# Performance work log

Hardware: AMD Instinct MI355X
Metric: run time of the kernel (lower is better)

## Reference

```python
import jax, jax.numpy as jnp
import numpy as np

B, N, K = 1, 100000, 16
C_IN, C_ADD, C_MID = 64, 16, 16
IN_F, OUT_F = (C_IN + C_ADD) * C_MID, 256


def setup_inputs() -> dict:
    key = jax.random.key(0)
    ks = jax.random.split(key, 8)
    return {
        "input_features": jax.random.normal(ks[0], (B, N, C_IN), dtype=jnp.float32),
        "neighbor_inds": jax.random.randint(ks[1], (B, N, K), 0, N, dtype=jnp.int32),
        "inverse_neighbors": jax.random.randint(ks[2], (B, N * K), 0, N, dtype=jnp.int32),
        "inverse_k": jax.random.randint(ks[3], (B, N + 1), 0, K, dtype=jnp.int32),
        "inverse_idx": jax.random.randint(ks[4], (B, N * K), 0, N * K, dtype=jnp.int32),
        "weightnet": jax.random.normal(ks[5], (B, N, K, C_MID), dtype=jnp.float32),
        "additional_features": jax.random.normal(ks[6], (B, N, K, C_ADD), dtype=jnp.float32),
        "linear_weights": jax.random.normal(ks[7], (OUT_F, IN_F), dtype=jnp.float32) * 0.02,
        "linear_bias": jnp.zeros((OUT_F,), dtype=jnp.float32),
    }


def reference(input_features, neighbor_inds, inverse_neighbors, inverse_k,
              inverse_idx, weightnet, additional_features,
              linear_weights, linear_bias):
    # Gather neighbor features: [B, N, K, C_in]
    gathered = jax.vmap(lambda f, idx: f[idx])(input_features, neighbor_inds)
    # Concatenate extra per-neighbor features: [B, N, K, C_in + C_add]
    feat = jnp.concatenate([gathered, additional_features], axis=-1)
    # WeightNet-weighted reduction over neighbors: [B, N, C, C_mid]
    pconv = jnp.einsum("bnkc,bnkm->bncm", feat, weightnet)
    pconv = pconv.reshape(pconv.shape[0], pconv.shape[1], -1)  # [B, N, C*C_mid]
    # Fused linear projection
    return pconv @ linear_weights.T + linear_bias
```

## Files before the change

kernel.cpp:

```cpp
#include <hip/hip_runtime.h>

#define NPTS 100000
#define PB 64
#define NBLK ((NPTS + PB - 1) / PB)
#define INF 1280
#define OUTF 256

using short8 = __attribute__((ext_vector_type(8))) short;
using f32x4  = __attribute__((ext_vector_type(4))) float;

__device__ __forceinline__ unsigned short f2bf(float x) {
  unsigned u = __float_as_uint(x);
  return (unsigned short)((u + 0x7FFFu + ((u >> 16) & 1u)) >> 16);
}

__global__ void k_prep(const float* __restrict__ in_f, unsigned short* __restrict__ inbf) {
  int i = blockIdx.x * 256 + threadIdx.x;
  if (i < 1600000) {
    float4 v = ((const float4*)in_f)[i];
    ushort4 o;
    o.x = f2bf(v.x); o.y = f2bf(v.y); o.z = f2bf(v.z); o.w = f2bf(v.w);
    ((ushort4*)inbf)[i] = o;
  }
}

__global__ void k_wconv(const float* __restrict__ W, unsigned short* __restrict__ Wb) {
  int g = blockIdx.x * 256 + threadIdx.x;
  int j = g & 7;
  int col = (g >> 3) & 15;
  int ks = (g >> 7) & 31;
  int rest = g >> 12;
  int ct = rest % 5, nt = rest / 5;
  int kh = ks * 8 + j;
  int m = kh >> 4, ci = kh & 15;
  Wb[g] = f2bf(W[(nt * 16 + col) * INF + (ct * 16 + ci) * 16 + m]);
}

__global__ __launch_bounds__(512, 4) void k_fused(
    const unsigned short* __restrict__ inbf, const int* __restrict__ nbr,
    const float* __restrict__ wn_g, const float* __restrict__ add_f,
    const unsigned short* __restrict__ Wb, const float* __restrict__ bias,
    float* __restrict__ out)
{
  __shared__ __align__(16) unsigned char sA[PB * 528];
  __shared__ __align__(16) unsigned char sW[PB * 512];
  __shared__ int s_nbr[PB * 16];

  const int t = threadIdx.x;
  const int w = t >> 6, lane = t & 63;
  const int g16 = lane >> 4;
  const int c16 = lane & 15;
  const long p0 = (long)blockIdx.x * PB;

  for (int i = t; i < PB * 16; i += 512) {
    long pp = p0 + (i >> 4); if (pp >= NPTS) pp = NPTS - 1;
    s_nbr[i] = nbr[pp * 16 + (i & 15)];
  }
#pragma unroll
  for (int it = 0; it < 8; ++it) {
    int flat4 = it * 512 + t;
    int p = flat4 >> 6, k = (flat4 >> 2) & 15, m4 = (flat4 & 3) * 4;
    long pp = p0 + p; if (pp >= NPTS) pp = NPTS - 1;
    float4 v = *(const float4*)(wn_g + pp * 256 + k * 16 + m4);
    unsigned short* wb = (unsigned short*)(sW + p * 512 + k * 2);
    wb[(m4 + 0) * 16] = f2bf(v.x);
    wb[(m4 + 1) * 16] = f2bf(v.y);
    wb[(m4 + 2) * 16] = f2bf(v.z);
    wb[(m4 + 3) * 16] = f2bf(v.w);
  }
  __syncthreads();

  f32x4 acc[2][4];
#pragma unroll
  for (int a = 0; a < 2; ++a)
#pragma unroll
    for (int b = 0; b < 4; ++b) acc[a][b] = (f32x4){0.f, 0.f, 0.f, 0.f};

  const int rt0 = (w & 1) * 2;
  const int nt0 = (w >> 1) * 4;

  for (int ct = 0; ct < 5; ++ct) {
#pragma unroll 2
    for (int i = 0; i < 8; ++i) {
      int p = w * 8 + i;
      long pp = p0 + p; if (pp >= NPTS) pp = NPTS - 1;
      short8 af = (short8){0, 0, 0, 0, 0, 0, 0, 0};
      short8 bf = (short8){0, 0, 0, 0, 0, 0, 0, 0};
      if (g16 < 2) {
        bf = *(const short8*)(sW + p * 512 + c16 * 32 + g16 * 16);
        int4 i0 = *(const int4*)&s_nbr[p * 16 + g16 * 8];
        int4 i1 = *(const int4*)&s_nbr[p * 16 + g16 * 8 + 4];
        unsigned short a8[8];
        if (ct < 4) {
          a8[0] = inbf[(long)i0.x * 64 + ct * 16 + c16];
          a8[1] = inbf[(long)i0.y * 64 + ct * 16 + c16];
          a8[2] = inbf[(long)i0.z * 64 + ct * 16 + c16];
          a8[3] = inbf[(long)i0.w * 64 + ct * 16 + c16];
          a8[4] = inbf[(long)i1.x * 64 + ct * 16 + c16];
          a8[5] = inbf[(long)i1.y * 64 + ct * 16 + c16];
          a8[6] = inbf[(long)i1.z * 64 + ct * 16 + c16];
          a8[7] = inbf[(long)i1.w * 64 + ct * 16 + c16];
        } else {
#pragma unroll
          for (int j = 0; j < 8; ++j)
            a8[j] = f2bf(add_f[(pp * 16 + g16 * 8 + j) * 16 + c16]);
        }
#pragma unroll
        for (int j = 0; j < 8; ++j) ((unsigned short*)&af)[j] = a8[j];
      }
      f32x4 d = __builtin_amdgcn_mfma_f32_16x16x32_bf16(af, bf, (f32x4){0.f, 0.f, 0.f, 0.f}, 0, 0, 0);
      unsigned lo = (unsigned)f2bf(d[0]) | ((unsigned)f2bf(d[1]) << 16);
      unsigned hi = (unsigned)f2bf(d[2]) | ((unsigned)f2bf(d[3]) << 16);
      *(uint2*)(sA + p * 528 + c16 * 32 + g16 * 8) = make_uint2(lo, hi);
    }
    __syncthreads();

#pragma unroll
    for (int kl = 0; kl < 8; ++kl) {
      short8 a0 = *(const short8*)(sA + (rt0 * 16 + c16) * 528 + kl * 64 + g16 * 16);
      short8 a1 = *(const short8*)(sA + ((rt0 + 1) * 16 + c16) * 528 + kl * 64 + g16 * 16);
#pragma unroll
      for (int ntl = 0; ntl < 4; ++ntl) {
        int nt = nt0 + ntl;
        short8 b = *(const short8*)(Wb + (((long)(nt * 5 + ct) * 32 + kl * 4 + g16) * 16 + c16) * 8);
        acc[0][ntl] = __builtin_amdgcn_mfma_f32_16x16x32_bf16(a0, b, acc[0][ntl], 0, 0, 0);
        acc[1][ntl] = __builtin_amdgcn_mfma_f32_16x16x32_bf16(a1, b, acc[1][ntl], 0, 0, 0);
      }
    }
    __syncthreads();
  }

#pragma unroll
  for (int ntl = 0; ntl < 4; ++ntl) {
    int n = nt0 * 16 + ntl * 16 + c16;
    float bv = bias[n];
#pragma unroll
    for (int rr = 0; rr < 2; ++rr) {
      long prow = p0 + (rt0 + rr) * 16 + g16 * 4;
#pragma unroll
      for (int r = 0; r < 4; ++r) {
        if (prow + r < NPTS) out[(prow + r) * 256 + n] = acc[rr][ntl][r] + bv;
      }
    }
  }
}

extern "C" void kernel_launch(void* const* d_in, const int* in_sizes, int n_in,
                              void* d_out, int out_size, void* d_ws, size_t ws_size,
                              hipStream_t stream) {
  const float* in_f  = (const float*)d_in[0];
  const int*   nbr   = (const int*)d_in[1];
  const float* wn    = (const float*)d_in[5];
  const float* add_f = (const float*)d_in[6];
  const float* W     = (const float*)d_in[7];
  const float* bias  = (const float*)d_in[8];
  float* out = (float*)d_out;

  unsigned short* inbf = (unsigned short*)d_ws;
  unsigned short* Wb   = (unsigned short*)((char*)d_ws + 13631488);

  k_prep<<<dim3(6250), dim3(256), 0, stream>>>(in_f, inbf);
  k_wconv<<<dim3(1280), dim3(256), 0, stream>>>(W, Wb);
  k_fused<<<dim3(NBLK), dim3(512), 0, stream>>>(inbf, nbr, wn, add_f, Wb, bias, out);
}
```

Baseline: 253.9 us.

## Prefetch next channel-tile gather into registers during GEMM with vectorized loads

Neighbor feature rows are now gathered with 16-byte vector loads into registers and staged through a transposed shared tile, instead of per-element 2-byte gathers. The gather for the next channel tile is issued before the current tile's GEMM, so gather latency overlaps with the MFMAs. Weightnet fragments are held in registers, and each wave now computes 4 row tiles by 2 output tiles rather than 2 by 4. The cost is more registers and shared-memory stores with 2-byte granularity.

New measurement: 254.3 us. Within noise of the previous version (+0.2%).

```diff
diff --git a/kernel.cpp b/kernel.cpp
--- a/kernel.cpp
+++ b/kernel.cpp
@@ -4,7 +4,7 @@
 #define PB 64
 #define NBLK ((NPTS + PB - 1) / PB)
 #define INF 1280
-#define OUTF 256
+#define PSTR 544
 
 using short8 = __attribute__((ext_vector_type(8))) short;
 using f32x4  = __attribute__((ext_vector_type(4))) float;
@@ -12,6 +12,9 @@
 __device__ __forceinline__ unsigned short f2bf(float x) {
   unsigned u = __float_as_uint(x);
   return (unsigned short)((u + 0x7FFFu + ((u >> 16) & 1u)) >> 16);
+}
+__device__ __forceinline__ unsigned pack2(float a, float b) {
+  return (unsigned)f2bf(a) | ((unsigned)f2bf(b) << 16);
 }
 
 __global__ void k_prep(const float* __restrict__ in_f, unsigned short* __restrict__ inbf) {
@@ -42,105 +45,154 @@
     const unsigned short* __restrict__ Wb, const float* __restrict__ bias,
     float* __restrict__ out)
 {
+  __shared__ __align__(16) unsigned char sF[PB * PSTR];
   __shared__ __align__(16) unsigned char sA[PB * 528];
-  __shared__ __align__(16) unsigned char sW[PB * 512];
-  __shared__ int s_nbr[PB * 16];
 
   const int t = threadIdx.x;
   const int w = t >> 6, lane = t & 63;
-  const int g16 = lane >> 4;
-  const int c16 = lane & 15;
+  const int g16 = lane >> 4, c16 = lane & 15;
   const long p0 = (long)blockIdx.x * PB;
 
-  for (int i = t; i < PB * 16; i += 512) {
-    long pp = p0 + (i >> 4); if (pp >= NPTS) pp = NPTS - 1;
-    s_nbr[i] = nbr[pp * 16 + (i & 15)];
-  }
-#pragma unroll
-  for (int it = 0; it < 8; ++it) {
-    int flat4 = it * 512 + t;
-    int p = flat4 >> 6, k = (flat4 >> 2) & 15, m4 = (flat4 & 3) * 4;
-    long pp = p0 + p; if (pp >= NPTS) pp = NPTS - 1;
-    float4 v = *(const float4*)(wn_g + pp * 256 + k * 16 + m4);
-    unsigned short* wb = (unsigned short*)(sW + p * 512 + k * 2);
-    wb[(m4 + 0) * 16] = f2bf(v.x);
-    wb[(m4 + 1) * 16] = f2bf(v.y);
-    wb[(m4 + 2) * 16] = f2bf(v.z);
-    wb[(m4 + 3) * 16] = f2bf(v.w);
-  }
-  __syncthreads();
-
-  f32x4 acc[2][4];
-#pragma unroll
-  for (int a = 0; a < 2; ++a)
-#pragma unroll
-    for (int b = 0; b < 4; ++b) acc[a][b] = (f32x4){0.f, 0.f, 0.f, 0.f};
-
-  const int rt0 = (w & 1) * 2;
-  const int nt0 = (w >> 1) * 4;
-
+  int uidx[4], upp[4];
+#pragma unroll
+  for (int i = 0; i < 4; ++i) {
+    int flat = i * 512 + t;
+    long pp = p0 + (flat >> 5); if (pp >= NPTS) pp = NPTS - 1;
+    upp[i] = (int)pp;
+    uidx[i] = nbr[pp * 16 + ((flat >> 1) & 15)];
+  }
+
+  uint4 sr[4];
+  auto gload = [&](int ct) {
+#pragma unroll
+    for (int i = 0; i < 4; ++i) {
+      int uh = (i * 512 + t) & 1;
+      sr[i] = *(const uint4*)(inbf + (long)uidx[i] * 64 + ct * 16 + uh * 8);
+    }
+  };
+  auto fload = [&]() {
+#pragma unroll
+    for (int i = 0; i < 4; ++i) {
+      int flat = i * 512 + t, uk = (flat >> 1) & 15, uh = flat & 1;
+      const float* s = add_f + (long)upp[i] * 256 + uk * 16 + uh * 8;
+      float4 a = *(const float4*)s, b = *(const float4*)(s + 4);
+      sr[i] = make_uint4(pack2(a.x, a.y), pack2(a.z, a.w), pack2(b.x, b.y), pack2(b.z, b.w));
+    }
+  };
+  auto swrite = [&]() {
+#pragma unroll
+    for (int i = 0; i < 4; ++i) {
+      int flat = i * 512 + t, up = flat >> 5, uk = (flat >> 1) & 15, uh = flat & 1;
+      unsigned char* base = sF + up * PSTR + uh * 256 + uk * 2;
+      *(unsigned short*)(base +   0) = (unsigned short)(sr[i].x);
+      *(unsigned short*)(base +  32) = (unsigned short)(sr[i].x >> 16);
+      *(unsigned short*)(base +  64) = (unsigned short)(sr[i].y);
+      *(unsigned short*)(base +  96) = (unsigned short)(sr[i].y >> 16);
+      *(unsigned short*)(base + 128) = (unsigned short)(sr[i].z);
+      *(unsigned short*)(base + 160) = (unsigned short)(sr[i].z >> 16);
+      *(unsigned short*)(base + 192) = (unsigned short)(sr[i].w);
+      *(unsigned short*)(base + 224) = (unsigned short)(sr[i].w >> 16);
+    }
+  };
+
+  gload(0);
+#pragma unroll
+  for (int i = 0; i < 4; ++i) {
+    int flat = i * 512 + t, up = flat >> 5, uk = (flat >> 1) & 15, uh = flat & 1;
+    const float* s = wn_g + (long)upp[i] * 256 + uk * 16 + uh * 8;
+    float4 a = *(const float4*)s, b = *(const float4*)(s + 4);
+    unsigned char* base = sF + up * PSTR + uh * 256 + uk * 2;
+    *(unsigned short*)(base +   0) = f2bf(a.x);
+    *(unsigned short*)(base +  32) = f2bf(a.y);
+    *(unsigned short*)(base +  64) = f2bf(a.z);
+    *(unsigned short*)(base +  96) = f2bf(a.w);
+    *(unsigned short*)(base + 128) = f2bf(b.x);
+    *(unsigned short*)(base + 160) = f2bf(b.y);
+    *(unsigned short*)(base + 192) = f2bf(b.z);
+    *(unsigned short*)(base + 224) = f2bf(b.w);
+  }
+  __syncthreads();
+
+  short8 bfr[8];
+#pragma unroll
+  for (int i = 0; i < 8; ++i) {
+    bfr[i] = (short8){0, 0, 0, 0, 0, 0, 0, 0};
+    if (g16 < 2)
+      bfr[i] = *(const short8*)(sF + (w * 8 + i) * PSTR + c16 * 32 + g16 * 16);
+  }
+  __syncthreads();
+
+  auto pconv = [&]() {
+#pragma unroll
+    for (int g = 0; g < 2; ++g) {
+      short8 af[4];
+#pragma unroll
+      for (int i = 0; i < 4; ++i) {
+        af[i] = (short8){0, 0, 0, 0, 0, 0, 0, 0};
+        if (g16 < 2)
+          af[i] = *(const short8*)(sF + (w * 8 + g * 4 + i) * PSTR + c16 * 32 + g16 * 16);
+      }
+#pragma unroll
+      for (int i = 0; i < 4; ++i) {
+        int p = w * 8 + g * 4 + i;
+        f32x4 d = __builtin_amdgcn_mfma_f32_16x16x32_bf16(
+            af[i], bfr[g * 4 + i], (f32x4){0.f, 0.f, 0.f, 0.f}, 0, 0, 0);
+        *(uint2*)(sA + p * 528 + c16 * 32 + g16 * 8) =
+            make_uint2(pack2(d[0], d[1]), pack2(d[2], d[3]));
+      }
+    }
+  };
+
+  f32x4 acc[4][2];
+#pragma unroll
+  for (int rr = 0; rr < 4; ++rr)
+#pragma unroll
+    for (int ntl = 0; ntl < 2; ++ntl) acc[rr][ntl] = (f32x4){0.f, 0.f, 0.f, 0.f};
+
+  auto gemm = [&](int ct) {
+#pragma unroll
+    for (int kl = 0; kl < 8; ++kl) {
+      short8 a[4];
+#pragma unroll
+      for (int rr = 0; rr < 4; ++rr)
+        a[rr] = *(const short8*)(sA + (rr * 16 + c16) * 528 + kl * 64 + g16 * 16);
+#pragma unroll
+      for (int ntl = 0; ntl < 2; ++ntl) {
+        int nt = w * 2 + ntl;
+        short8 b = *(const short8*)(Wb + ((long)((nt * 5 + ct) * 32 + kl * 4 + g16) * 16 + c16) * 8);
+#pragma unroll
+        for (int rr = 0; rr < 4; ++rr)
+          acc[rr][ntl] = __builtin_amdgcn_mfma_f32_16x16x32_bf16(a[rr], b, acc[rr][ntl], 0, 0, 0);
+      }
+    }
+  };
+
+  swrite();
+  __syncthreads();
+  pconv();
+  __syncthreads();
   for (int ct = 0; ct < 5; ++ct) {
-#pragma unroll 2
-    for (int i = 0; i < 8; ++i) {
-      int p = w * 8 + i;
-      long pp = p0 + p; if (pp >= NPTS) pp = NPTS - 1;
-      short8 af = (short8){0, 0, 0, 0, 0, 0, 0, 0};
-      short8 bf = (short8){0, 0, 0, 0, 0, 0, 0, 0};
-      if (g16 < 2) {
-        bf = *(const short8*)(sW + p * 512 + c16 * 32 + g16 * 16);
-        int4 i0 = *(const int4*)&s_nbr[p * 16 + g16 * 8];
-        int4 i1 = *(const int4*)&s_nbr[p * 16 + g16 * 8 + 4];
-        unsigned short a8[8];
-        if (ct < 4) {
-          a8[0] = inbf[(long)i0.x * 64 + ct * 16 + c16];
-          a8[1] = inbf[(long)i0.y * 64 + ct * 16 + c16];
-          a8[2] = inbf[(long)i0.z * 64 + ct * 16 + c16];
-          a8[3] = inbf[(long)i0.w * 64 + ct * 16 + c16];
-          a8[4] = inbf[(long)i1.x * 64 + ct * 16 + c16];
-          a8[5] = inbf[(long)i1.y * 64 + ct * 16 + c16];
-          a8[6] = inbf[(long)i1.z * 64 + ct * 16 + c16];
-          a8[7] = inbf[(long)i1.w * 64 + ct * 16 + c16];
-        } else {
-#pragma unroll
-          for (int j = 0; j < 8; ++j)
-            a8[j] = f2bf(add_f[(pp * 16 + g16 * 8 + j) * 16 + c16]);
-        }
-#pragma unroll
-        for (int j = 0; j < 8; ++j) ((unsigned short*)&af)[j] = a8[j];
-      }
-      f32x4 d = __builtin_amdgcn_mfma_f32_16x16x32_bf16(af, bf, (f32x4){0.f, 0.f, 0.f, 0.f}, 0, 0, 0);
-      unsigned lo = (unsigned)f2bf(d[0]) | ((unsigned)f2bf(d[1]) << 16);
-      unsigned hi = (unsigned)f2bf(d[2]) | ((unsigned)f2bf(d[3]) << 16);
-      *(uint2*)(sA + p * 528 + c16 * 32 + g16 * 8) = make_uint2(lo, hi);
-    }
-    __syncthreads();
-
-#pragma unroll
-    for (int kl = 0; kl < 8; ++kl) {
-      short8 a0 = *(const short8*)(sA + (rt0 * 16 + c16) * 528 + kl * 64 + g16 * 16);
-      short8 a1 = *(const short8*)(sA + ((rt0 + 1) * 16 + c16) * 528 + kl * 64 + g16 * 16);
-#pragma unroll
-      for (int ntl = 0; ntl < 4; ++ntl) {
-        int nt = nt0 + ntl;
-        short8 b = *(const short8*)(Wb + (((long)(nt * 5 + ct) * 32 + kl * 4 + g16) * 16 + c16) * 8);
-        acc[0][ntl] = __builtin_amdgcn_mfma_f32_16x16x32_bf16(a0, b, acc[0][ntl], 0, 0, 0);
-        acc[1][ntl] = __builtin_amdgcn_mfma_f32_16x16x32_bf16(a1, b, acc[1][ntl], 0, 0, 0);
-      }
-    }
-    __syncthreads();
-  }
-
-#pragma unroll
-  for (int ntl = 0; ntl < 4; ++ntl) {
-    int n = nt0 * 16 + ntl * 16 + c16;
+    if (ct < 3) gload(ct + 1);
+    else if (ct == 3) fload();
+    gemm(ct);
+    if (ct < 4) {
+      swrite();
+      __syncthreads();
+      pconv();
+      __syncthreads();
+    }
+  }
+
+#pragma unroll
+  for (int ntl = 0; ntl < 2; ++ntl) {
+    int n = (w * 2 + ntl) * 16 + c16;
     float bv = bias[n];
 #pragma unroll
-    for (int rr = 0; rr < 2; ++rr) {
-      long prow = p0 + (rt0 + rr) * 16 + g16 * 4;
-#pragma unroll
-      for (int r = 0; r < 4; ++r) {
+    for (int rr = 0; rr < 4; ++rr) {
+      long prow = p0 + rr * 16 + g16 * 4;
+#pragma unroll
+      for (int r = 0; r < 4; ++r)
         if (prow + r < NPTS) out[(prow + r) * 256 + n] = acc[rr][ntl][r] + bv;
-      }
     }
   }
 }
```
